# Kernel tuning notes

Measured on AMD Instinct MI355X. Metric: run time of the kernel, lower is better.

The kernel has to match this reference:

```python
import jax, jax.numpy as jnp
import numpy as np

B, N, DIM, H, D, S = 4, 16384, 256, 8, 64, 64
INNER = H * D


def setup_inputs() -> dict:
    key = jax.random.key(0)
    ks = jax.random.split(key, 10)
    f = lambda k, shp, s: jax.random.normal(k, shp, jnp.float32) * s
    return {
        "x": jax.random.normal(ks[0], (B, N, DIM), jnp.float32),
        "Wx": f(ks[1], (INNER, DIM), 0.02), "bx": jnp.zeros((INNER,), jnp.float32),
        "Wfx": f(ks[2], (INNER, DIM), 0.02), "bfx": jnp.zeros((INNER,), jnp.float32),
        "Wslice": f(ks[3], (S, D), 0.125), "bslice": jnp.zeros((S,), jnp.float32),
        "temperature": jnp.full((1, H, 1, 1), 0.5, jnp.float32),
        "Wq": f(ks[4], (D, D), 0.125),
        "Wk": f(ks[5], (D, D), 0.125),
        "Wv": f(ks[6], (D, D), 0.125),
        "attn_scale": jnp.full((1, H, 1, 1), 10.0, jnp.float32),
        "slice_res_scale": jnp.full((1,), 0.1, jnp.float32),
        "Wout": f(ks[7], (DIM, INNER), 0.02), "bout": jnp.zeros((DIM,), jnp.float32),
    }


def reference(x, Wx, bx, Wfx, bfx, Wslice, bslice, temperature,
              Wq, Wk, Wv, attn_scale, slice_res_scale, Wout, bout):
    b, n, _ = x.shape
    # project and split heads -> [b, h, n, d]
    fx = (x @ Wfx.T + bfx).reshape(b, n, H, D).transpose(0, 2, 1, 3)
    xm = (x @ Wx.T + bx).reshape(b, n, H, D).transpose(0, 2, 1, 3)
    temp = jnp.clip(temperature, 1e-4)
    slice_logits = (xm @ Wslice.T + bslice) / temp              # [b,h,n,S]
    w = jax.nn.softmax(slice_logits, axis=-1)                   # slice weights
    slice_norm = w.sum(axis=2)                                  # [b,h,S]
    tok = jnp.einsum('bhnc,bhng->bhgc', fx, w)                  # [b,h,S,d]
    tok = tok / (slice_norm + 1e-5)[:, :, :, None]
    # small cross-slice attention (cosine, shared kv across heads)
    q = tok @ Wq.T                                              # [b,h,S,d]
    kv = tok.mean(axis=1, keepdims=True)                        # [b,1,S,d]
    k = kv @ Wk.T
    v = kv @ Wv.T
    qn = q / jnp.maximum(jnp.linalg.norm(q, axis=-1, keepdims=True), 1e-12)
    kn = k / jnp.maximum(jnp.linalg.norm(k, axis=-1, keepdims=True), 1e-12)
    logits = jnp.einsum('bhgd,bzsd->bhgs', qn, kn) * attn_scale  # z==1 broadcast
    attn = jax.nn.softmax(logits, axis=-1)
    out_tok = jnp.einsum('bhgs,bzsd->bhgd', attn, v)
    out_tok = out_tok + slice_res_scale * tok
    # broadcast slice tokens back to points
    out_x = jnp.einsum('bhgc,bhng->bhnc', out_tok, w)           # [b,h,n,d]
    out_x = out_x.transpose(0, 2, 1, 3).reshape(b, n, H * D)
    return out_x @ Wout.T + bout
```

## Files before the change

### kernel.cpp

```cpp
#include <hip/hip_runtime.h>
#include <math.h>

#define BQ   4
#define NTOK 16384
#define DIMM 256
#define HH   8
#define DDIM 64
#define SSL  64
#define INNERD 512
#define BN_TOK (BQ*NTOK)

typedef __attribute__((ext_vector_type(8))) short short8;
typedef __attribute__((ext_vector_type(4))) float f32x4;

__device__ inline float bf2f(unsigned short u) {
    union { float f; unsigned int i; } v; v.i = ((unsigned int)u) << 16; return v.f;
}
__device__ inline unsigned short f2bf(float f) {
    union { float f; unsigned int i; } v; v.f = f;
    unsigned int r = v.i + 0x7FFFu + ((v.i >> 16) & 1u);
    return (unsigned short)(r >> 16);
}

__device__ __forceinline__ void gl_lds16(const void* g, void* l) {
    __builtin_amdgcn_global_load_lds(
        (const __attribute__((address_space(1))) unsigned int*)g,
        (__attribute__((address_space(3))) unsigned int*)l, 16, 0, 0);
}

__global__ void k_prep(const float* __restrict__ Wx, const float* __restrict__ bx,
                       const float* __restrict__ Wfx, const float* __restrict__ bfx,
                       const float* __restrict__ Wslice, const float* __restrict__ bslice,
                       unsigned short* __restrict__ Wcatb, float* __restrict__ bcat)
{
    int row = blockIdx.x;
    int t = threadIdx.x;
    if (row < 512) {
        for (int c = t; c < 256; c += 64) Wcatb[row*256 + c] = f2bf(Wfx[row*256 + c]);
        if (t == 0) bcat[row] = bfx[row];
    } else {
        int r = row - 512, h = r >> 6, s = r & 63;
        for (int c = t; c < 256; c += 64) {
            float acc = 0.f;
            for (int d = 0; d < 64; ++d)
                acc += Wslice[s*64 + d] * Wx[(h*64 + d)*256 + c];
            Wcatb[row*256 + c] = f2bf(acc);
        }
        if (t == 0) {
            float acc = bslice[s];
            for (int d = 0; d < 64; ++d) acc += Wslice[s*64 + d] * bx[h*64 + d];
            bcat[row] = acc;
        }
    }
}

__global__ void k_xcast(const float* __restrict__ x, unsigned short* __restrict__ xb)
{
    size_t i = ((size_t)blockIdx.x*256 + threadIdx.x)*8;
    float4 a = *(const float4*)(x + i);
    float4 b = *(const float4*)(x + i + 4);
    *(ushort4*)(xb + i)     = make_ushort4(f2bf(a.x), f2bf(a.y), f2bf(a.z), f2bf(a.w));
    *(ushort4*)(xb + i + 4) = make_ushort4(f2bf(b.x), f2bf(b.y), f2bf(b.z), f2bf(b.w));
}

__global__ __launch_bounds__(256) void k_gemm1(
    const unsigned short* __restrict__ Xb, const unsigned short* __restrict__ Wb,
    const float* __restrict__ bias, const float* __restrict__ temperature,
    unsigned short* __restrict__ fx_t, unsigned short* __restrict__ wbuf)
{
    __shared__ unsigned short As[2][128*32];
    __shared__ unsigned short Bs[2][128*32];
    int bid = blockIdx.x;
    int xcd = bid & 7;
    int inner = bid >> 3;
    int rt = xcd*64 + (inner >> 3);
    int ct = inner & 7;
    int m0 = rt*128, n0 = ct*128;
    int tid = threadIdx.x;
    int lane = tid & 63, w = tid >> 6;
    int wr = w >> 1, wc = w & 1;
    int lr = lane & 15, lq = lane >> 4;

    f32x4 acc[4][4];
#pragma unroll
    for (int i = 0; i < 4; i++)
#pragma unroll
        for (int j = 0; j < 4; j++) acc[i][j] = (f32x4)(0.f);

    int r0 = tid >> 2, kq0 = (tid & 3) * 8;

    auto stage = [&](int buf, int k0) {
        gl_lds16(Xb + (size_t)(m0 + r0)*256 + k0 + kq0,      &As[buf][(size_t)tid*8]);
        gl_lds16(Xb + (size_t)(m0 + 64 + r0)*256 + k0 + kq0, &As[buf][(size_t)(tid+256)*8]);
        gl_lds16(Wb + (size_t)(n0 + r0)*256 + k0 + kq0,      &Bs[buf][(size_t)tid*8]);
        gl_lds16(Wb + (size_t)(n0 + 64 + r0)*256 + k0 + kq0, &Bs[buf][(size_t)(tid+256)*8]);
    };

    stage(0, 0);
    __syncthreads();
    int cur = 0;
    for (int k0 = 0; k0 < 256; k0 += 32) {
        short8 af[4], bf[4];
#pragma unroll
        for (int i = 0; i < 4; i++) {
            af[i] = *(const short8*)&As[cur][(wr*64 + i*16 + lr)*32 + lq*8];
            bf[i] = *(const short8*)&Bs[cur][(wc*64 + i*16 + lr)*32 + lq*8];
        }
        if (k0 + 32 < 256) stage(cur ^ 1, k0 + 32);
#pragma unroll
        for (int i = 0; i < 4; i++)
#pragma unroll
            for (int j = 0; j < 4; j++)
                acc[i][j] = __builtin_amdgcn_mfma_f32_16x16x32_bf16(af[i], bf[j], acc[i][j], 0, 0, 0);
        __syncthreads();
        cur ^= 1;
    }

    float bv[4];
#pragma unroll
    for (int j = 0; j < 4; j++) bv[j] = bias[n0 + wc*64 + j*16 + lr];

    if (n0 < 512) {
        int h = (n0 + wc*64) >> 6;
        int batch = m0 >> 14;
#pragma unroll
        for (int i = 0; i < 4; i++) {
            int tokbase = m0 + wr*64 + i*16 + lq*4;
            int nloc = tokbase & (NTOK-1);
#pragma unroll
            for (int j = 0; j < 4; j++) {
                int d = j*16 + lr;
                ushort4 pk = make_ushort4(
                    f2bf(acc[i][j][0] + bv[j]), f2bf(acc[i][j][1] + bv[j]),
                    f2bf(acc[i][j][2] + bv[j]), f2bf(acc[i][j][3] + bv[j]));
                *(ushort4*)(fx_t + ((size_t)(batch*8 + h)*64 + d)*NTOK + nloc) = pk;
            }
        }
    } else {
        int h = (n0 - 512 + wc*64) >> 6;
        float it = 1.f / fmaxf(temperature[h], 1e-4f);
        int colbase = (n0 - 512) + wc*64;
#pragma unroll
        for (int i = 0; i < 4; i++) {
            int tokbase = m0 + wr*64 + i*16 + lq*4;
#pragma unroll
            for (int r = 0; r < 4; r++) {
                float v[4];
#pragma unroll
                for (int j = 0; j < 4; j++) v[j] = (acc[i][j][r] + bv[j]) * it;
                float mx = fmaxf(fmaxf(v[0], v[1]), fmaxf(v[2], v[3]));
                mx = fmaxf(mx, __shfl_xor(mx, 1));
                mx = fmaxf(mx, __shfl_xor(mx, 2));
                mx = fmaxf(mx, __shfl_xor(mx, 4));
                mx = fmaxf(mx, __shfl_xor(mx, 8));
                float e[4], sm = 0.f;
#pragma unroll
                for (int j = 0; j < 4; j++) { e[j] = __expf(v[j] - mx); sm += e[j]; }
                sm += __shfl_xor(sm, 1);
                sm += __shfl_xor(sm, 2);
                sm += __shfl_xor(sm, 4);
                sm += __shfl_xor(sm, 8);
                float inv = 1.f / sm;
                size_t rowoff = (size_t)(tokbase + r)*512 + colbase + lr;
#pragma unroll
                for (int j = 0; j < 4; j++)
                    wbuf[rowoff + j*16] = f2bf(e[j] * inv);
            }
        }
    }
}

__global__ __launch_bounds__(256) void k_tok(
    const unsigned short* __restrict__ wbuf, const unsigned short* __restrict__ fx_t,
    float* __restrict__ tok_acc, float* __restrict__ norm_acc)
{
    __shared__ unsigned short As[2][32*64];
    __shared__ unsigned short Bs[2][64*32];
    int chunk = blockIdx.x;
    int bh = blockIdx.y;
    int b = bh >> 3, h = bh & 7;
    int n0 = chunk * 512;
    int tid = threadIdx.x;
    int lane = tid & 63, w = tid >> 6;
    int lr = lane & 15, lq = lane >> 4;

    f32x4 acc[4];
#pragma unroll
    for (int j = 0; j < 4; j++) acc[j] = (f32x4)(0.f);
    float nacc = 0.f;

    const unsigned short* wsrc =
        wbuf + ((size_t)(b*NTOK + n0 + (tid >> 3)))*512 + h*64 + (tid & 7)*8;
    const unsigned short* fsrc =
        fx_t + ((size_t)bh*64 + (tid >> 2))*NTOK + n0 + (tid & 3)*8;

    auto stage = [&](int buf, int kk) {
        gl_lds16(wsrc + (size_t)kk*512, &As[buf][(size_t)tid*8]);
        gl_lds16(fsrc + kk,             &Bs[buf][(size_t)tid*8]);
    };

    stage(0, 0);
    __syncthreads();
    int cur = 0;
    for (int kk = 0; kk < 512; kk += 32) {
        const unsigned short* arow = &As[cur][w*16 + lr];
        short8 af;
        float ns = 0.f;
#pragma unroll
        for (int e = 0; e < 8; ++e) {
            unsigned short u = arow[(lq*8 + e)*64];
            af[e] = (short)u;
            ns += bf2f(u);
        }
        short8 bfv[4];
#pragma unroll
        for (int j = 0; j < 4; j++)
            bfv[j] = *(const short8*)&Bs[cur][(j*16 + lr)*32 + lq*8];

        if (kk + 32 < 512) stage(cur ^ 1, kk + 32);

        nacc += ns;
#pragma unroll
        for (int j = 0; j < 4; j++)
            acc[j] = __builtin_amdgcn_mfma_f32_16x16x32_bf16(af, bfv[j], acc[j], 0, 0, 0);

        __syncthreads();
        cur ^= 1;
    }

#pragma unroll
    for (int j = 0; j < 4; j++) {
        int d = j*16 + lr;
#pragma unroll
        for (int r = 0; r < 4; r++) {
            int s = w*16 + lq*4 + r;
            atomicAdd(&tok_acc[((size_t)bh*64 + s)*64 + d], acc[j][r]);
        }
    }
    nacc += __shfl_xor(nacc, 16);
    nacc += __shfl_xor(nacc, 32);
    if (lq == 0)
        atomicAdd(&norm_acc[bh*64 + w*16 + lr], nacc);
}

__global__ __launch_bounds__(256) void k_kv(
    const float* __restrict__ tok, const float* __restrict__ norm,
    const float* __restrict__ Wk, const float* __restrict__ Wv,
    float* __restrict__ kn_out, float* __restrict__ v_out)
{
    __shared__ float KV[64][65];
    __shared__ float TMP[64][65];
    __shared__ float rn[64];
    __shared__ float inv[8][64];
    int b = blockIdx.x, tid = threadIdx.x;
    for (int idx = tid; idx < 512; idx += 256) {
        int h = idx >> 6, s = idx & 63;
        inv[h][s] = 1.f / (norm[(b*8 + h)*64 + s] + 1e-5f);
    }
    __syncthreads();
    for (int idx = tid; idx < 4096; idx += 256) {
        int s = idx >> 6;
        float acc = 0.f;
        for (int h = 0; h < 8; ++h)
            acc += tok[((size_t)(b*8 + h))*4096 + idx] * inv[h][s];
        KV[s][idx & 63] = acc * 0.125f;
    }
    __syncthreads();
    for (int idx = tid; idx < 4096; idx += 256) {
        int s = idx >> 6, d = idx & 63;
        float a = 0.f;
        for (int e = 0; e < 64; ++e) a += KV[s][e] * Wk[d*64 + e];
        TMP[s][d] = a;
    }
    __syncthreads();
    if (tid < 64) {
        float a = 0.f;
        for (int d = 0; d < 64; ++d) { float x = TMP[tid][d]; a += x*x; }
        rn[tid] = fmaxf(sqrtf(a), 1e-12f);
    }
    __syncthreads();
    for (int idx = tid; idx < 4096; idx += 256) {
        int s = idx >> 6, d = idx & 63;
        kn_out[(size_t)b*4096 + idx] = TMP[s][d] / rn[s];
    }
    for (int idx = tid; idx < 4096; idx += 256) {
        int s = idx >> 6, d = idx & 63;
        float a = 0.f;
        for (int e = 0; e < 64; ++e) a += KV[s][e] * Wv[d*64 + e];
        v_out[(size_t)b*4096 + idx] = a;
    }
}

__global__ __launch_bounds__(256) void k_attn(
    const float* __restrict__ tok, const float* __restrict__ norm,
    const float* __restrict__ Wq,
    const float* __restrict__ kn, const float* __restrict__ vbuf,
    const float* __restrict__ attn_scale, const float* __restrict__ srs,
    float* __restrict__ out_tok)
{
    __shared__ float TN[64][65];
    __shared__ float Q[64][65];
    __shared__ float KN[64][65];
    __shared__ float L[64][65];
    __shared__ float rn[64];
    int h = blockIdx.x & 7, b = blockIdx.x >> 3;
    int bh = b*8 + h;
    int tid = threadIdx.x;
    for (int idx = tid; idx < 4096; idx += 256) {
        int g = idx >> 6;
        TN[g][idx & 63] = tok[(size_t)bh*4096 + idx] / (norm[bh*64 + g] + 1e-5f);
        KN[g][idx & 63] = kn[(size_t)b*4096 + idx];
    }
    __syncthreads();
    for (int idx = tid; idx < 4096; idx += 256) {
        int g = idx >> 6, d = idx & 63;
        float a = 0.f;
        for (int e = 0; e < 64; ++e) a += TN[g][e] * Wq[d*64 + e];
        Q[g][d] = a;
    }
    __syncthreads();
    if (tid < 64) {
        float a = 0.f;
        for (int d = 0; d < 64; ++d) { float x = Q[tid][d]; a += x*x; }
        rn[tid] = fmaxf(sqrtf(a), 1e-12f);
    }
    __syncthreads();
    float scale = attn_scale[h];
    for (int idx = tid; idx < 4096; idx += 256) {
        int g = idx >> 6, s = idx & 63;
        float a = 0.f;
        for (int e = 0; e < 64; ++e) a += Q[g][e] * KN[s][e];
        L[g][s] = a / rn[g] * scale;
    }
    __syncthreads();
    if (tid < 64) {
        float mx = -1e30f;
        for (int s = 0; s < 64; ++s) mx = fmaxf(mx, L[tid][s]);
        float sm = 0.f;
        for (int s = 0; s < 64; ++s) { float e = expf(L[tid][s]-mx); L[tid][s] = e; sm += e; }
        float ivv = 1.f/sm;
        for (int s = 0; s < 64; ++s) L[tid][s] *= ivv;
    }
    __syncthreads();
    float srsv = srs[0];
    for (int idx = tid; idx < 4096; idx += 256) {
        int g = idx >> 6, d = idx & 63;
        float a = 0.f;
        for (int s = 0; s < 64; ++s) a += L[g][s] * vbuf[(size_t)b*4096 + s*64 + d];
        out_tok[(size_t)bh*4096 + idx] = a + srsv * TN[g][d];
    }
}

__global__ __launch_bounds__(256) void k_mt(
    const float* __restrict__ out_tok, const float* __restrict__ Wout,
    unsigned short* __restrict__ MTb)
{
    __shared__ float Wt[64][68];
    __shared__ float Ot[64][68];
    int jt = blockIdx.x, h = blockIdx.y, b = blockIdx.z;
    int j0 = jt * 64;
    int tid = threadIdx.x;
    int tx = tid & 15, ty = tid >> 4;
#pragma unroll
    for (int i = 0; i < 4; i++) {
        int flat = tid + i*256;
        int r = flat >> 4;
        int c4 = (flat & 15) * 4;
        float4 wv = *(const float4*)(Wout + (size_t)(j0+r)*512 + h*64 + c4);
        Wt[c4+0][r]=wv.x; Wt[c4+1][r]=wv.y; Wt[c4+2][r]=wv.z; Wt[c4+3][r]=wv.w;
        float4 ov = *(const float4*)(out_tok + ((size_t)(b*8+h)*64 + r)*64 + c4);
        Ot[c4+0][r]=ov.x; Ot[c4+1][r]=ov.y; Ot[c4+2][r]=ov.z; Ot[c4+3][r]=ov.w;
    }
    __syncthreads();
    float acc[4][4] = {{0.f}};
#pragma unroll 8
    for (int d = 0; d < 64; ++d) {
        float av[4], bv[4];
        *(float4*)av = *(const float4*)&Wt[d][ty*4];
        *(float4*)bv = *(const float4*)&Ot[d][tx*4];
#pragma unroll
        for (int i = 0; i < 4; i++)
#pragma unroll
            for (int j = 0; j < 4; j++) acc[i][j] += av[i]*bv[j];
    }
#pragma unroll
    for (int i = 0; i < 4; i++) {
        int j = j0 + ty*4 + i;
#pragma unroll
        for (int jj = 0; jj < 4; jj++) {
            int s = tx*4 + jj;
            MTb[((size_t)(b*256) + j)*512 + h*64 + s] = f2bf(acc[i][jj]);
        }
    }
}

__global__ __launch_bounds__(256) void k_gemm2(
    const unsigned short* __restrict__ A, const unsigned short* __restrict__ Ball,
    const float* __restrict__ bias, float* __restrict__ C)
{
    __shared__ unsigned short As[2][128*32];
    __shared__ unsigned short Bs[2][128*32];
    int bid = blockIdx.x;
    int xcd = bid & 7;
    int inner = bid >> 3;
    int rt = xcd*64 + (inner >> 1);
    int ct = inner & 1;
    int m0 = rt*128, n0 = ct*128;
    const unsigned short* Bm = Ball + (size_t)(m0 >> 14) * 256 * 512;
    int tid = threadIdx.x;
    int lane = tid & 63, w = tid >> 6;
    int wr = w >> 1, wc = w & 1;
    int lr = lane & 15, lq = lane >> 4;

    f32x4 acc[4][4];
#pragma unroll
    for (int i = 0; i < 4; i++)
#pragma unroll
        for (int j = 0; j < 4; j++) acc[i][j] = (f32x4)(0.f);

    int r0 = tid >> 2, kq0 = (tid & 3) * 8;

    auto stage = [&](int buf, int k0) {
        gl_lds16(A + (size_t)(m0 + r0)*512 + k0 + kq0,       &As[buf][(size_t)tid*8]);
        gl_lds16(A + (size_t)(m0 + 64 + r0)*512 + k0 + kq0,  &As[buf][(size_t)(tid+256)*8]);
        gl_lds16(Bm + (size_t)(n0 + r0)*512 + k0 + kq0,      &Bs[buf][(size_t)tid*8]);
        gl_lds16(Bm + (size_t)(n0 + 64 + r0)*512 + k0 + kq0, &Bs[buf][(size_t)(tid+256)*8]);
    };

    stage(0, 0);
    __syncthreads();
    int cur = 0;
    for (int k0 = 0; k0 < 512; k0 += 32) {
        short8 af[4], bf[4];
#pragma unroll
        for (int i = 0; i < 4; i++) {
            af[i] = *(const short8*)&As[cur][(wr*64 + i*16 + lr)*32 + lq*8];
            bf[i] = *(const short8*)&Bs[cur][(wc*64 + i*16 + lr)*32 + lq*8];
        }
        if (k0 + 32 < 512) stage(cur ^ 1, k0 + 32);
#pragma unroll
        for (int i = 0; i < 4; i++)
#pragma unroll
            for (int j = 0; j < 4; j++)
                acc[i][j] = __builtin_amdgcn_mfma_f32_16x16x32_bf16(af[i], bf[j], acc[i][j], 0, 0, 0);
        __syncthreads();
        cur ^= 1;
    }

#pragma unroll
    for (int j = 0; j < 4; j++) {
        int n = n0 + wc*64 + j*16 + lr;
        float bv = bias[n];
#pragma unroll
        for (int i = 0; i < 4; i++) {
            int mrow = m0 + wr*64 + i*16 + lq*4;
#pragma unroll
            for (int r = 0; r < 4; r++)
                C[(size_t)(mrow + r)*256 + n] = acc[i][j][r] + bv;
        }
    }
}

extern "C" void kernel_launch(void* const* d_in, const int* in_sizes, int n_in,
                              void* d_out, int out_size, void* d_ws, size_t ws_size,
                              hipStream_t stream)
{
    const float* x      = (const float*)d_in[0];
    const float* Wx     = (const float*)d_in[1];
    const float* bx     = (const float*)d_in[2];
    const float* Wfx    = (const float*)d_in[3];
    const float* bfx    = (const float*)d_in[4];
    const float* Wslice = (const float*)d_in[5];
    const float* bslice = (const float*)d_in[6];
    const float* temperature = (const float*)d_in[7];
    const float* Wq     = (const float*)d_in[8];
    const float* Wk     = (const float*)d_in[9];
    const float* Wv     = (const float*)d_in[10];
    const float* attn_scale = (const float*)d_in[11];
    const float* srs    = (const float*)d_in[12];
    const float* Wout   = (const float*)d_in[13];
    const float* bout   = (const float*)d_in[14];
    float* out = (float*)d_out;
    float* ws  = (float*)d_ws;

    float* tok  = ws + 0;
    float* norm = ws + 131072;
    float* bcat = ws + 133120;
    float* kn   = ws + 134144;
    float* vb   = ws + 150528;
    float* ot   = ws + 166912;
    unsigned short* Wcatb = (unsigned short*)(ws + 297984);
    unsigned short* MTb   = (unsigned short*)(ws + 429056);
    unsigned short* xb    = (unsigned short*)(ws + 691200);
    unsigned short* wbuf  = (unsigned short*)(ws + 9079808);
    unsigned short* fx_t  = (unsigned short*)d_out;

    hipMemsetAsync(tok, 0, 133120 * sizeof(float), stream);
    k_prep<<<1024, 64, 0, stream>>>(Wx, bx, Wfx, bfx, Wslice, bslice, Wcatb, bcat);
    k_xcast<<<8192, 256, 0, stream>>>(x, xb);
    k_gemm1<<<4096, 256, 0, stream>>>(xb, Wcatb, bcat, temperature, fx_t, wbuf);
    k_tok<<<dim3(32, 32), 256, 0, stream>>>(wbuf, fx_t, tok, norm);
    k_kv<<<4, 256, 0, stream>>>(tok, norm, Wk, Wv, kn, vb);
    k_attn<<<32, 256, 0, stream>>>(tok, norm, Wq, kn, vb, attn_scale, srs, ot);
    k_mt<<<dim3(4, 8, 4), 256, 0, stream>>>(ot, Wout, MTb);
    k_gemm2<<<1024, 256, 0, stream>>>(wbuf, MTb, bout, out);
}
```

Baseline: 370.4 us.

## Prefetch two K-tiles ahead with explicit vmcnt waits in all three GEMM loops

Rewrites the double-buffered LDS loops in the projection GEMM, the slice-token reduction GEMM and the output GEMM so that two stages are in flight before the loop starts. Each iteration now waits only on the oldest outstanding global-to-LDS loads via s_waitcnt vmcnt, and the loops are fully unrolled. After the fragment reads, a second barrier lets the current buffer be refilled with tile t+2. The goal is to hide global load latency behind MFMA work and drop the full __syncthreads drain. The risk is that the hand-written waitcnt counts and barriers are fragile, and the extra barrier per iteration adds sync cost.

```diff
diff --git a/kernel.cpp b/kernel.cpp
--- a/kernel.cpp
+++ b/kernel.cpp
@@ -27,6 +27,9 @@
         (const __attribute__((address_space(1))) unsigned int*)g,
         (__attribute__((address_space(3))) unsigned int*)l, 16, 0, 0);
 }
+
+#define WAIT_VM(N) asm volatile("s_waitcnt vmcnt(" #N ")" ::: "memory")
+#define WAIT_LGKM0() asm volatile("s_waitcnt lgkmcnt(0)" ::: "memory")
 
 __global__ void k_prep(const float* __restrict__ Wx, const float* __restrict__ bx,
                        const float* __restrict__ Wfx, const float* __restrict__ bfx,
@@ -97,22 +100,27 @@
     };
 
     stage(0, 0);
-    __syncthreads();
+    stage(1, 32);
     int cur = 0;
-    for (int k0 = 0; k0 < 256; k0 += 32) {
+#pragma unroll
+    for (int t = 0; t < 8; ++t) {
+        if (t < 7) { WAIT_VM(4); } else { WAIT_VM(0); }
+        __builtin_amdgcn_s_barrier();
         short8 af[4], bf[4];
 #pragma unroll
         for (int i = 0; i < 4; i++) {
             af[i] = *(const short8*)&As[cur][(wr*64 + i*16 + lr)*32 + lq*8];
             bf[i] = *(const short8*)&Bs[cur][(wc*64 + i*16 + lr)*32 + lq*8];
         }
-        if (k0 + 32 < 256) stage(cur ^ 1, k0 + 32);
+        WAIT_LGKM0();
+        __builtin_amdgcn_sched_barrier(0);
+        __builtin_amdgcn_s_barrier();
+        if (t < 6) stage(cur, (t + 2) * 32);
 #pragma unroll
         for (int i = 0; i < 4; i++)
 #pragma unroll
             for (int j = 0; j < 4; j++)
                 acc[i][j] = __builtin_amdgcn_mfma_f32_16x16x32_bf16(af[i], bf[j], acc[i][j], 0, 0, 0);
-        __syncthreads();
         cur ^= 1;
     }
 
@@ -200,31 +208,33 @@
     };
 
     stage(0, 0);
-    __syncthreads();
+    stage(1, 32);
     int cur = 0;
-    for (int kk = 0; kk < 512; kk += 32) {
+#pragma unroll
+    for (int t = 0; t < 16; ++t) {
+        if (t < 15) { WAIT_VM(2); } else { WAIT_VM(0); }
+        __builtin_amdgcn_s_barrier();
         const unsigned short* arow = &As[cur][w*16 + lr];
         short8 af;
-        float ns = 0.f;
-#pragma unroll
-        for (int e = 0; e < 8; ++e) {
-            unsigned short u = arow[(lq*8 + e)*64];
-            af[e] = (short)u;
-            ns += bf2f(u);
-        }
+#pragma unroll
+        for (int e = 0; e < 8; ++e)
+            af[e] = (short)arow[(lq*8 + e)*64];
         short8 bfv[4];
 #pragma unroll
         for (int j = 0; j < 4; j++)
             bfv[j] = *(const short8*)&Bs[cur][(j*16 + lr)*32 + lq*8];
-
-        if (kk + 32 < 512) stage(cur ^ 1, kk + 32);
-
+        WAIT_LGKM0();
+        __builtin_amdgcn_sched_barrier(0);
+        __builtin_amdgcn_s_barrier();
+        if (t < 14) stage(cur, (t + 2) * 32);
+
+        float ns = 0.f;
+#pragma unroll
+        for (int e = 0; e < 8; ++e) ns += bf2f((unsigned short)af[e]);
         nacc += ns;
 #pragma unroll
         for (int j = 0; j < 4; j++)
             acc[j] = __builtin_amdgcn_mfma_f32_16x16x32_bf16(af, bfv[j], acc[j], 0, 0, 0);
-
-        __syncthreads();
         cur ^= 1;
     }
 
@@ -428,22 +438,27 @@
     };
 
     stage(0, 0);
-    __syncthreads();
+    stage(1, 32);
     int cur = 0;
-    for (int k0 = 0; k0 < 512; k0 += 32) {
+#pragma unroll
+    for (int t = 0; t < 16; ++t) {
+        if (t < 15) { WAIT_VM(4); } else { WAIT_VM(0); }
+        __builtin_amdgcn_s_barrier();
         short8 af[4], bf[4];
 #pragma unroll
         for (int i = 0; i < 4; i++) {
             af[i] = *(const short8*)&As[cur][(wr*64 + i*16 + lr)*32 + lq*8];
             bf[i] = *(const short8*)&Bs[cur][(wc*64 + i*16 + lr)*32 + lq*8];
         }
-        if (k0 + 32 < 512) stage(cur ^ 1, k0 + 32);
+        WAIT_LGKM0();
+        __builtin_amdgcn_sched_barrier(0);
+        __builtin_amdgcn_s_barrier();
+        if (t < 14) stage(cur, (t + 2) * 32);
 #pragma unroll
         for (int i = 0; i < 4; i++)
 #pragma unroll
             for (int j = 0; j < 4; j++)
                 acc[i][j] = __builtin_amdgcn_mfma_f32_16x16x32_bf16(af[i], bf[j], acc[i][j], 0, 0, 0);
-        __syncthreads();
         cur ^= 1;
     }
 
```

After: 368.7 us. No clear change (-0.5%).
